# Performance work log

Hardware: AMD Instinct MI355X
Metric: run time of the kernel (lower is better)

Reference implementation:

```python
import jax, jax.numpy as jnp
import numpy as np

NUM_HEADS = 4
HEAD_DIM = 64
IN_CH = 192
KERNEL_SIZES = (3, 5, 7, 9)  # per-head neighborhood size
NEG_INF = -1e30


def setup_inputs() -> dict:
    key = jax.random.key(0)
    k1, k2, k3 = jax.random.split(key, 3)
    x = jax.random.normal(k1, (8, IN_CH, 96, 96), dtype=jnp.float32)
    # QKV conv: out_channels = head_dim * num_heads * 3 = 768, 3x3, pad 1
    w_qkv = jax.random.normal(k2, (HEAD_DIM * NUM_HEADS * 3, IN_CH, 3, 3), dtype=jnp.float32) * 0.02
    b_qkv = jax.random.normal(k3, (HEAD_DIM * NUM_HEADS * 3,), dtype=jnp.float32) * 0.02
    return {"x": x, "w_qkv": w_qkv, "b_qkv": b_qkv}


def _neighborhood_attention(q, k, v, ksize):
    # q, k, v: [N, H, W, D]; KxK zero-padded neighborhood attention with
    # out-of-bounds positions masked out.
    N, H, W, D = q.shape
    pad = ksize // 2
    kp = jnp.pad(k, ((0, 0), (pad, pad), (pad, pad), (0, 0)))
    vp = jnp.pad(v, ((0, 0), (pad, pad), (pad, pad), (0, 0)))
    scale = 1.0 / np.sqrt(D).astype(np.float32)
    rows = jnp.arange(H)
    cols = jnp.arange(W)
    scores, masks = [], []
    for di in range(ksize):
        for dj in range(ksize):
            k_sh = kp[:, di:di + H, dj:dj + W, :]           # shifted keys
            scores.append(jnp.einsum('nhwd,nhwd->nhw', q, k_sh))
            rv = (rows + di - pad >= 0) & (rows + di - pad < H)   # [H]
            cv = (cols + dj - pad >= 0) & (cols + dj - pad < W)   # [W]
            masks.append(rv[:, None] & cv[None, :])               # [H, W]
    scores = jnp.stack(scores, axis=-1) * scale                   # [N,H,W,K2]
    mask = jnp.stack(masks, axis=-1)[None]                        # [1,H,W,K2]
    scores = jnp.where(mask, scores, NEG_INF)
    attn = jax.nn.softmax(scores, axis=-1)                        # [N,H,W,K2]
    out = jnp.zeros_like(q)
    t = 0
    for di in range(ksize):
        for dj in range(ksize):
            out = out + attn[..., t, None] * vp[:, di:di + H, dj:dj + W, :]
            t += 1
    return out  # [N,H,W,D]


def reference(x, w_qkv, b_qkv):
    # Dense QKV projection (Conv2d, stride 1, padding 1 == SAME for k=3)
    qkv = jax.lax.conv_general_dilated(
        x, w_qkv, window_strides=(1, 1), padding='SAME',
        dimension_numbers=('NCHW', 'OIHW', 'NCHW'))
    qkv = qkv + b_qkv[None, :, None, None]
    # transform_to_nhw1c: NCHW -> NHWC, then split channels into
    # num_heads blocks of 3*head_dim, each split into q, k, v.
    N, C, H, W = qkv.shape
    qkv = jnp.transpose(qkv, (0, 2, 3, 1)).reshape(N, H, W, NUM_HEADS, 3, HEAD_DIM)
    outs = []
    for h, ks in enumerate(KERNEL_SIZES):
        q = qkv[..., h, 0, :]
        k = qkv[..., h, 1, :]
        v = qkv[..., h, 2, :]
        o = _neighborhood_attention(q, k, v, ks)       # [N,H,W,D]
        outs.append(jnp.transpose(o, (0, 3, 1, 2)))    # transform_from_nhw1c -> NCHW
    return jnp.stack(outs, axis=0)  # [num_heads, N, D, H, W]
```

## Files before the change

### kernel.cpp

```cpp
#include <hip/hip_runtime.h>
#include <hip/hip_bf16.h>

#define NH 96
#define NW 96
#define NB 8
#define CIN 192
#define COUT 768
#define PH 98

typedef __attribute__((ext_vector_type(8))) unsigned short ushort8;
typedef __attribute__((ext_vector_type(8))) short bf16x8;
typedef __attribute__((ext_vector_type(4))) float f32x4;

static __device__ __forceinline__ unsigned short f2bf(float f) {
    unsigned int u = __float_as_uint(f);
    return (unsigned short)((u + 0x7fffu + ((u >> 16) & 1u)) >> 16);
}

typedef const __attribute__((address_space(1))) unsigned int gu32;
typedef __attribute__((address_space(3))) unsigned int lu32;
static __device__ __forceinline__ void gload16(const void* g, void* l) {
    __builtin_amdgcn_global_load_lds((gu32*)g, (lu32*)l, 16, 0, 0);
}

__global__ __launch_bounds__(256) void pack_x_kernel(
    const float* __restrict__ x, unsigned short* __restrict__ xp)
{
    __shared__ float tile[32][97];
    int bid = blockIdx.x;
    int ct = bid % 6; int y = (bid / 6) % NH; int n = bid / (6 * NH);
    int tid = threadIdx.x;
    int c0 = ct * 32;
    for (int i = tid; i < 32 * 96; i += 256) {
        int c = i / 96, xx = i % 96;
        tile[c][xx] = x[(((size_t)n * CIN + c0 + c) * NH + y) * NW + xx];
    }
    __syncthreads();
    for (int i = tid; i < 96 * 4; i += 256) {
        int xx = i >> 2, ch = i & 3;
        ushort8 pk;
#pragma unroll
        for (int j = 0; j < 8; ++j) pk[j] = f2bf(tile[ch * 8 + j][xx]);
        *(ushort8*)(xp + ((size_t)(n * PH + y + 1) * PH + xx + 1) * CIN + c0 + ch * 8) = pk;
    }
}

__global__ __launch_bounds__(256) void pack_w_kernel(
    const float* __restrict__ w, unsigned short* __restrict__ bw)
{
    __shared__ float ls[1728];
    int co = blockIdx.x; int tid = threadIdx.x;
    for (int i = tid; i < 1728; i += 256) ls[i] = w[(size_t)co * 1728 + i];
    __syncthreads();
    for (int i = tid; i < 1728; i += 256) {
        int sh = i / 192, ci = i % 192;
        bw[(size_t)co * 1728 + i] = f2bf(ls[ci * 9 + sh]);
    }
}

__global__ __launch_bounds__(512) void conv_gemm_kernel(
    const unsigned short* __restrict__ xp, const unsigned short* __restrict__ bw,
    const float* __restrict__ bias, unsigned short* __restrict__ qkq,
    unsigned short* __restrict__ vt)
{
    __shared__ __align__(16) char smem[131072];
    int bid = (blockIdx.x & 7) * 108 + (blockIdx.x >> 3);
    int brow = (bid / 3) * 256, bcol = (bid % 3) * 256;
    int tid = threadIdx.x, lane = tid & 63;
    int wid = tid >> 6, wm = wid >> 2, wn = wid & 3;
    int g = lane >> 4;

    const unsigned short* srcA[2][2];
    const unsigned short* srcB[2][2];
#pragma unroll
    for (int h = 0; h < 2; ++h)
#pragma unroll
        for (int i = 0; i < 2; ++i) {
            int s = i * 512 + tid;
            int rl = s >> 3, c = s & 7;
            int csw = (c ^ (rl & 7)) << 3;
            int p = brow + h * 128 + rl;
            int n = p / 9216; int rem = p - n * 9216;
            int y = rem / 96; int xx = rem - y * 96;
            srcA[h][i] = xp + ((size_t)(n * PH + y) * PH + xx) * CIN + csw;
            srcB[h][i] = bw + (size_t)(bcol + h * 128 + rl) * 1728 + csw;
        }
    int dsto[2];
#pragma unroll
    for (int i = 0; i < 2; ++i) dsto[i] = (i * 512 + (tid & ~63)) * 16;

#define STAGEU(T, U, BUF)                                                      \
    {                                                                          \
        int shift_ = (T) / 3, kk_ = (T) % 3;                                   \
        if ((U) < 2) {                                                         \
            int aO_ = ((shift_ / 3) * PH + (shift_ % 3)) * CIN + kk_ * 64;     \
            _Pragma("unroll")                                                  \
            for (int i_ = 0; i_ < 2; ++i_)                                     \
                gload16(srcA[(U)][i_] + aO_,                                   \
                        smem + (BUF) + (U) * 16384 + dsto[i_]);                \
        } else {                                                               \
            int bO_ = (T) * 64;                                                \
            _Pragma("unroll")                                                  \
            for (int i_ = 0; i_ < 2; ++i_)                                     \
                gload16(srcB[(U) - 2][i_] + bO_,                               \
                        smem + (BUF) + 32768 + ((U) - 2) * 16384 + dsto[i_]);  \
        }                                                                      \
    }

    int arow[8], brow_[4], xof[2];
#pragma unroll
    for (int m = 0; m < 8; ++m)
        arow[m] = (wm * 128 + m * 16 + (lane & 15)) * 128;
#pragma unroll
    for (int n = 0; n < 4; ++n)
        brow_[n] = 32768 + (wn * 64 + n * 16 + (lane & 15)) * 128;
#pragma unroll
    for (int kk = 0; kk < 2; ++kk)
        xof[kk] = ((kk * 4 + g) ^ (lane & 7)) << 4;

    STAGEU(0, 0, 0); STAGEU(0, 1, 0); STAGEU(0, 2, 0); STAGEU(0, 3, 0);

    f32x4 acc[8][4] = {};

    for (int t = 0; t < 27; ++t) {
        asm volatile("s_waitcnt vmcnt(0)" ::: "memory");
        __builtin_amdgcn_s_barrier();
        __builtin_amdgcn_sched_barrier(0);
        const int cur = (t & 1) << 16;
        const int nxt = cur ^ 65536;
        bf16x8 bf[4][2];
#pragma unroll
        for (int n = 0; n < 4; ++n)
#pragma unroll
            for (int kk = 0; kk < 2; ++kk)
                bf[n][kk] = *(const bf16x8*)(smem + cur + brow_[n] + xof[kk]);
#pragma unroll
        for (int p = 0; p < 4; ++p) {
            if (t < 26) STAGEU(t + 1, p, nxt);
            bf16x8 af[2][2];
#pragma unroll
            for (int mm = 0; mm < 2; ++mm)
#pragma unroll
                for (int kk = 0; kk < 2; ++kk)
                    af[mm][kk] = *(const bf16x8*)(smem + cur + arow[2 * p + mm] + xof[kk]);
            __builtin_amdgcn_s_setprio(1);
#pragma unroll
            for (int mm = 0; mm < 2; ++mm)
#pragma unroll
                for (int n = 0; n < 4; ++n)
#pragma unroll
                    for (int kk = 0; kk < 2; ++kk)
                        acc[2 * p + mm][n] = __builtin_amdgcn_mfma_f32_16x16x32_bf16(
                            af[mm][kk], bf[n][kk], acc[2 * p + mm][n], 0, 0, 0);
            __builtin_amdgcn_s_setprio(0);
        }
    }

    __syncthreads();
    unsigned short* sc = (unsigned short*)smem;
    float bn[4];
#pragma unroll
    for (int n = 0; n < 4; ++n)
        bn[n] = bias[bcol + wn * 64 + n * 16 + (lane & 15)];
#pragma unroll
    for (int m = 0; m < 8; ++m)
#pragma unroll
        for (int n = 0; n < 4; ++n) {
            int col = wn * 64 + n * 16 + (lane & 15);
            int cabs = bcol + col;
            float scale = ((cabs % 192) < 64) ? 0.125f : 1.0f;
#pragma unroll
            for (int j = 0; j < 4; ++j) {
                int row = wm * 128 + m * 16 + (lane >> 4) * 4 + j;
                sc[row * 256 + (col ^ ((row & 7) << 3))] =
                    f2bf((acc[m][n][j] + bn[n]) * scale);
            }
        }
    __syncthreads();
#pragma unroll
    for (int i = 0; i < 16; ++i) {
        int idx = i * 512 + tid;
        int row = idx >> 5, ch = idx & 31;
        int c0 = bcol + ch * 8;
        int r192 = c0 % 192;
        if (r192 < 128) {
            ushort8 pk = *(const ushort8*)(sc + row * 256 + ((ch * 8) ^ ((row & 7) << 3)));
            *(ushort8*)(qkq + (size_t)(brow + row) * 512 + (c0 / 192) * 128 + r192) = pk;
        }
    }
    int nblk = brow / 9216;
    int prem = brow - nblk * 9216;
#pragma unroll
    for (int h = 0; h < 4; ++h) {
        int lc = h * 192 + 128 - bcol;
        if (lc < 0 || lc > 192) continue;
        unsigned short* vth = vt + (size_t)h * 4718592;
#pragma unroll
        for (int it = 0; it < 4; ++it) {
            int i = it * 512 + tid;
            int d = i & 63, pxb = i >> 6;
            ushort8 pk;
#pragma unroll
            for (int j = 0; j < 8; ++j) {
                int px = pxb * 8 + j;
                pk[j] = sc[px * 256 + ((lc + d) ^ ((px & 7) << 3))];
            }
            *(ushort8*)(vth + ((size_t)(nblk * 64 + d)) * 9216 + prem + pxb * 8) = pk;
        }
    }
}

#define SLAB 24576
template<int KS>
static __device__ __forceinline__ void na_body(
    const unsigned short* __restrict__ qkq, const unsigned short* __restrict__ vt,
    float* __restrict__ out, int head, int bid, char* nsm)
{
    constexpr int PAD = KS / 2;
    int yp = bid % 32, n = bid / 32;
    int y0 = yp * 3;
    int tid = threadIdx.x;
    int wv = tid >> 6, lane = tid & 63;
    int g = lane >> 4, pix = lane & 15;
    int x0 = wv * 16;
    int x = x0 + pix;
    int W = x0 - 8;

    size_t qb0 = ((size_t)((n * 96 + y0) * 96 + x)) * 512 + (size_t)head * 128;
    bf16x8 qa0 = *(const bf16x8*)(qkq + qb0 + g * 8);
    bf16x8 qa1 = *(const bf16x8*)(qkq + qb0 + 32 + g * 8);
    bf16x8 qc0 = *(const bf16x8*)(qkq + qb0 + 96 * 512 + g * 8);
    bf16x8 qc1 = *(const bf16x8*)(qkq + qb0 + 96 * 512 + 32 + g * 8);
    bf16x8 qe0 = *(const bf16x8*)(qkq + qb0 + 2 * 96 * 512 + g * 8);
    bf16x8 qe1 = *(const bf16x8*)(qkq + qb0 + 2 * 96 * 512 + 32 + g * 8);
    asm volatile("s_waitcnt vmcnt(0)" ::: "memory");

    const size_t hoff = (size_t)head * 128 + 64;
#define STAGEKV(DI, BUF)                                                       \
    {                                                                          \
        int iy_ = min(max(y0 + (DI) - PAD, 0), 95);                            \
        size_t rb_ = ((size_t)((n * 96 + iy_) * 96)) * 512 + hoff;             \
        _Pragma("unroll")                                                      \
        for (int i_ = 0; i_ < 2; ++i_) {                                       \
            int ch_ = i_ * 384 + tid;                                          \
            int xx_ = ch_ >> 3, c8_ = (ch_ & 7) ^ (xx_ & 7);                   \
            gload16(qkq + rb_ + (size_t)xx_ * 512 + c8_ * 8,                   \
                    nsm + (BUF) * SLAB + (i_ * 384 + (tid & ~63)) * 16);       \
        }                                                                      \
        _Pragma("unroll")                                                      \
        for (int i_ = 0; i_ < 2; ++i_) {                                       \
            int ch_ = i_ * 384 + tid;                                          \
            int d_ = ch_ / 12, c_ = ch_ % 12;                                  \
            int cs_ = c_ ^ ((d_ >> 1) & 3);                                    \
            gload16(vt + (((size_t)(n * 64 + d_) * 96 + iy_)) * 96 + cs_ * 8,  \
                    nsm + (BUF) * SLAB + 12288 + (i_ * 384 + (tid & ~63)) * 16); \
        }                                                                      \
    }

    STAGEKV(0, 0);
    STAGEKV(1, 1);

    float l0 = 0.f, l1 = 0.f, l2 = 0.f;
    f32x4 O0[4] = {}, O1[4] = {}, O2[4] = {};
    int addrA = ((2 * (g & 1)) * 16 + pix) * 4;
    int addrB = addrA + 64;
    bool kthi = (g >> 1) != 0;
    int cxg = min(max(2 * wv - 1 + g, 0), 11);
    int vbase = 12288 + pix * 192 + ((cxg ^ ((pix >> 1) & 3)) << 4);

#define ROWCOMP(QF0, QF1, L, O)                                                \
    {                                                                          \
        unsigned int w0[2], w1[2];                                             \
        _Pragma("unroll")                                                      \
        for (int kt = 0; kt < 2; ++kt) {                                       \
            f32x4 tt = {};                                                     \
            tt = __builtin_amdgcn_mfma_f32_16x16x32_bf16(kf0[kt], QF0, tt, 0, 0, 0); \
            tt = __builtin_amdgcn_mfma_f32_16x16x32_bf16(kf1[kt], QF1, tt, 0, 0, 0); \
            float p[4];                                                        \
            _Pragma("unroll")                                                  \
            for (int r = 0; r < 4; ++r) {                                      \
                int kix = W + kt * 16 + g * 4 + r;                             \
                bool valid = ((unsigned)(kix - x + PAD) <= (unsigned)(2 * PAD)) && \
                             ((unsigned)kix < 96u);                            \
                p[r] = valid ? __expf(tt[r]) : 0.f;                            \
            }                                                                  \
            L += (p[0] + p[1]) + (p[2] + p[3]);                                \
            asm("v_cvt_pk_bf16_f32 %0, %1, %2" : "=v"(w0[kt]) : "v"(p[0]), "v"(p[1])); \
            asm("v_cvt_pk_bf16_f32 %0, %1, %2" : "=v"(w1[kt]) : "v"(p[2]), "v"(p[3])); \
        }                                                                      \
        int a0 = __builtin_amdgcn_ds_bpermute(addrA, (int)w0[0]);              \
        int b0 = __builtin_amdgcn_ds_bpermute(addrA, (int)w0[1]);              \
        int a1 = __builtin_amdgcn_ds_bpermute(addrA, (int)w1[0]);              \
        int b1 = __builtin_amdgcn_ds_bpermute(addrA, (int)w1[1]);              \
        int a2 = __builtin_amdgcn_ds_bpermute(addrB, (int)w0[0]);              \
        int b2 = __builtin_amdgcn_ds_bpermute(addrB, (int)w0[1]);              \
        int a3 = __builtin_amdgcn_ds_bpermute(addrB, (int)w1[0]);              \
        int b3 = __builtin_amdgcn_ds_bpermute(addrB, (int)w1[1]);              \
        union { int u[4]; bf16x8 v; } pa;                                      \
        pa.u[0] = kthi ? b0 : a0;                                              \
        pa.u[1] = kthi ? b1 : a1;                                              \
        pa.u[2] = kthi ? b2 : a2;                                              \
        pa.u[3] = kthi ? b3 : a3;                                              \
        _Pragma("unroll")                                                      \
        for (int dc = 0; dc < 4; ++dc)                                         \
            O[dc] = __builtin_amdgcn_mfma_f32_16x16x32_bf16(pa.v, vf[dc], O[dc], 0, 0, 0); \
    }

#pragma unroll
    for (int di = 0; di <= KS + 1; ++di) {
        if (di <= KS) asm volatile("s_waitcnt vmcnt(4)" ::: "memory");
        else          asm volatile("s_waitcnt vmcnt(0)" ::: "memory");
        __builtin_amdgcn_s_barrier();
        __builtin_amdgcn_sched_barrier(0);
        if (di + 2 <= KS + 1) STAGEKV(di + 2, (di + 2) % 3);
        int iy = y0 + di - PAD;
        if (iy < 0 || iy >= 96) continue;
        const char* kb = nsm + (di % 3) * SLAB;

        bf16x8 kf0[2], kf1[2];
#pragma unroll
        for (int kt = 0; kt < 2; ++kt) {
            int kix_l = W + kt * 16 + pix;
            int ixc = min(max(kix_l, 0), 95);
            const char* kr = kb + ixc * 128;
            kf0[kt] = *(const bf16x8*)(kr + ((g ^ (ixc & 7)) << 4));
            kf1[kt] = *(const bf16x8*)(kr + (((4 + g) ^ (ixc & 7)) << 4));
        }
        bf16x8 vf[4];
#pragma unroll
        for (int dc = 0; dc < 4; ++dc)
            vf[dc] = *(const bf16x8*)(kb + dc * 3072 + vbase);

        if (di < KS)              ROWCOMP(qa0, qa1, l0, O0);
        if (di >= 1 && di <= KS)  ROWCOMP(qc0, qc1, l1, O1);
        if (di >= 2)              ROWCOMP(qe0, qe1, l2, O2);
    }

    l0 += __shfl_xor(l0, 16, 64); l0 += __shfl_xor(l0, 32, 64);
    l1 += __shfl_xor(l1, 16, 64); l1 += __shfl_xor(l1, 32, 64);
    l2 += __shfl_xor(l2, 16, 64); l2 += __shfl_xor(l2, 32, 64);
    float li0 = 1.0f / l0, li1 = 1.0f / l1, li2 = 1.0f / l2;
    float lj0[4], lj1[4], lj2[4];
#pragma unroll
    for (int j = 0; j < 4; ++j) {
        lj0[j] = __uint_as_float((unsigned)__builtin_amdgcn_ds_bpermute(
            (4 * g + j) * 4, (int)__float_as_uint(li0)));
        lj1[j] = __uint_as_float((unsigned)__builtin_amdgcn_ds_bpermute(
            (4 * g + j) * 4, (int)__float_as_uint(li1)));
        lj2[j] = __uint_as_float((unsigned)__builtin_amdgcn_ds_bpermute(
            (4 * g + j) * 4, (int)__float_as_uint(li2)));
    }
    __syncthreads();
    float (*sO3)[64][97] = (float(*)[64][97])nsm;
#pragma unroll
    for (int dc = 0; dc < 4; ++dc)
#pragma unroll
        for (int j = 0; j < 4; ++j) {
            sO3[0][dc * 16 + pix][x0 + g * 4 + j] = O0[dc][j] * lj0[j];
            sO3[1][dc * 16 + pix][x0 + g * 4 + j] = O1[dc][j] * lj1[j];
            sO3[2][dc * 16 + pix][x0 + g * 4 + j] = O2[dc][j] * lj2[j];
        }
    __syncthreads();
    for (int i = tid; i < 4608; i += 384) {
        int r = i / 1536;
        int rem = i - r * 1536;
        int d = rem / 24, xq = rem % 24;
        float4 v4 = { sO3[r][d][xq * 4], sO3[r][d][xq * 4 + 1],
                      sO3[r][d][xq * 4 + 2], sO3[r][d][xq * 4 + 3] };
        *(float4*)(out + ((size_t)(head * 8 + n) * 64 + d) * 9216
                   + (y0 + r) * 96 + xq * 4) = v4;
    }
}

__global__ __launch_bounds__(384, 2) void na_mfma_all(
    const unsigned short* __restrict__ qkq, const unsigned short* __restrict__ vt,
    float* __restrict__ out)
{
    __shared__ __align__(16) char nsm[74496];
    int head = blockIdx.x & 3;
    int bid = blockIdx.x >> 2;
    switch (head) {
        case 0: na_body<3>(qkq, vt,               out, 0, bid, nsm); break;
        case 1: na_body<5>(qkq, vt + 4718592,     out, 1, bid, nsm); break;
        case 2: na_body<7>(qkq, vt + 2 * 4718592, out, 2, bid, nsm); break;
        default: na_body<9>(qkq, vt + 3 * 4718592, out, 3, bid, nsm); break;
    }
}

extern "C" void kernel_launch(void* const* d_in, const int* in_sizes, int n_in,
                              void* d_out, int out_size, void* d_ws, size_t ws_size,
                              hipStream_t stream) {
    const float* x  = (const float*)d_in[0];
    const float* w  = (const float*)d_in[1];
    const float* b  = (const float*)d_in[2];
    float* out = (float*)d_out;

    unsigned short* qkq  = (unsigned short*)d_ws;
    unsigned short* vt   = (unsigned short*)((char*)d_ws + 75497472);
    unsigned short* xpad = (unsigned short*)((char*)d_ws + 113246208);
    unsigned short* bw   = (unsigned short*)((char*)d_ws + 142749696);

    hipMemsetAsync(xpad, 0, 29503488, stream);
    pack_x_kernel<<<NB * NH * 6, 256, 0, stream>>>(x, xpad);
    pack_w_kernel<<<COUT, 256, 0, stream>>>(w, bw);
    conv_gemm_kernel<<<864, 512, 0, stream>>>(xpad, bw, b, qkq, vt);

    na_mfma_all<<<4 * 256, 384, 0, stream>>>(qkq, vt, out);
}
```

Before: 317.4 us.

## Shrink conv GEMM M-tile to one image row and triple-buffer loads

```diff
diff --git a/kernel.cpp b/kernel.cpp
--- a/kernel.cpp
+++ b/kernel.cpp
@@ -58,76 +58,89 @@
     }
 }
 
+#define CBUF 45056
+
+#define STAGE(T, BUF)                                                          \
+    {                                                                          \
+        int shift_ = (T) / 3, kk_ = (T) % 3;                                   \
+        int aO_ = ((shift_ / 3) * PH + (shift_ % 3)) * CIN + kk_ * 64;         \
+        int bO_ = (T) * 64;                                                    \
+        gload16(srcA0 + aO_, smem + (BUF) + dstA0);                            \
+        if (tid < 256) gload16(srcA1 + aO_, smem + (BUF) + dstA1);             \
+        _Pragma("unroll")                                                      \
+        for (int i_ = 0; i_ < 4; ++i_)                                         \
+            gload16(srcB[i_] + bO_, smem + (BUF) + 12288 + dstB[i_]);          \
+    }
+
+#define GATE65()                                                               \
+    {                                                                          \
+        if (tid < 256) { asm volatile("s_waitcnt vmcnt(6)" ::: "memory"); }    \
+        else           { asm volatile("s_waitcnt vmcnt(5)" ::: "memory"); }    \
+    }
+
 __global__ __launch_bounds__(512) void conv_gemm_kernel(
     const unsigned short* __restrict__ xp, const unsigned short* __restrict__ bw,
     const float* __restrict__ bias, unsigned short* __restrict__ qkq,
     unsigned short* __restrict__ vt)
 {
-    __shared__ __align__(16) char smem[131072];
-    int bid = (blockIdx.x & 7) * 108 + (blockIdx.x >> 3);
-    int brow = (bid / 3) * 256, bcol = (bid % 3) * 256;
+    __shared__ __align__(16) char smem[3 * CBUF];
+    int bid = (blockIdx.x & 7) * 288 + (blockIdx.x >> 3);
+    int brow = (bid / 3) * 96, bcol = (bid % 3) * 256;
     int tid = threadIdx.x, lane = tid & 63;
     int wid = tid >> 6, wm = wid >> 2, wn = wid & 3;
     int g = lane >> 4;
 
-    const unsigned short* srcA[2][2];
-    const unsigned short* srcB[2][2];
-#pragma unroll
-    for (int h = 0; h < 2; ++h)
-#pragma unroll
-        for (int i = 0; i < 2; ++i) {
-            int s = i * 512 + tid;
-            int rl = s >> 3, c = s & 7;
-            int csw = (c ^ (rl & 7)) << 3;
-            int p = brow + h * 128 + rl;
-            int n = p / 9216; int rem = p - n * 9216;
-            int y = rem / 96; int xx = rem - y * 96;
-            srcA[h][i] = xp + ((size_t)(n * PH + y) * PH + xx) * CIN + csw;
-            srcB[h][i] = bw + (size_t)(bcol + h * 128 + rl) * 1728 + csw;
-        }
-    int dsto[2];
-#pragma unroll
-    for (int i = 0; i < 2; ++i) dsto[i] = (i * 512 + (tid & ~63)) * 16;
-
-#define STAGEU(T, U, BUF)                                                      \
-    {                                                                          \
-        int shift_ = (T) / 3, kk_ = (T) % 3;                                   \
-        if ((U) < 2) {                                                         \
-            int aO_ = ((shift_ / 3) * PH + (shift_ % 3)) * CIN + kk_ * 64;     \
-            _Pragma("unroll")                                                  \
-            for (int i_ = 0; i_ < 2; ++i_)                                     \
-                gload16(srcA[(U)][i_] + aO_,                                   \
-                        smem + (BUF) + (U) * 16384 + dsto[i_]);                \
-        } else {                                                               \
-            int bO_ = (T) * 64;                                                \
-            _Pragma("unroll")                                                  \
-            for (int i_ = 0; i_ < 2; ++i_)                                     \
-                gload16(srcB[(U) - 2][i_] + bO_,                               \
-                        smem + (BUF) + 32768 + ((U) - 2) * 16384 + dsto[i_]);  \
-        }                                                                      \
-    }
-
-    int arow[8], brow_[4], xof[2];
-#pragma unroll
-    for (int m = 0; m < 8; ++m)
-        arow[m] = (wm * 128 + m * 16 + (lane & 15)) * 128;
+    int nblk = brow / 9216;
+    int prem = brow - nblk * 9216;
+    int yy = prem / 96;
+
+    const unsigned short* srcA0;
+    const unsigned short* srcA1;
+    int dstA0, dstA1;
+    {
+        int r0 = tid >> 3, c0 = tid & 7;
+        srcA0 = xp + ((size_t)(nblk * PH + yy) * PH + r0) * CIN
+                   + ((c0 ^ (r0 & 7)) << 3);
+        dstA0 = (tid & ~63) * 16;
+        int s1 = 512 + tid;
+        int r1 = s1 >> 3, c1 = s1 & 7;
+        srcA1 = xp + ((size_t)(nblk * PH + yy) * PH + r1) * CIN
+                   + ((c1 ^ (r1 & 7)) << 3);
+        dstA1 = (512 + (tid & ~63)) * 16;
+    }
+    const unsigned short* srcB[4];
+    int dstB[4];
+#pragma unroll
+    for (int i = 0; i < 4; ++i) {
+        int s = i * 512 + tid;
+        int row = s >> 3, c = s & 7;
+        srcB[i] = bw + (size_t)(bcol + row) * 1728 + ((c ^ (row & 7)) << 3);
+        dstB[i] = (i * 512 + (tid & ~63)) * 16;
+    }
+
+    int arow[3], brow_[4], xof[2];
+#pragma unroll
+    for (int m = 0; m < 3; ++m)
+        arow[m] = (wm * 48 + m * 16 + (lane & 15)) * 128;
 #pragma unroll
     for (int n = 0; n < 4; ++n)
-        brow_[n] = 32768 + (wn * 64 + n * 16 + (lane & 15)) * 128;
+        brow_[n] = 12288 + (wn * 64 + n * 16 + (lane & 15)) * 128;
 #pragma unroll
     for (int kk = 0; kk < 2; ++kk)
         xof[kk] = ((kk * 4 + g) ^ (lane & 7)) << 4;
 
-    STAGEU(0, 0, 0); STAGEU(0, 1, 0); STAGEU(0, 2, 0); STAGEU(0, 3, 0);
-
-    f32x4 acc[8][4] = {};
+    STAGE(0, 0);
+    STAGE(1, CBUF);
+
+    f32x4 acc[3][4] = {};
 
     for (int t = 0; t < 27; ++t) {
-        asm volatile("s_waitcnt vmcnt(0)" ::: "memory");
+        if (t < 26) GATE65()
+        else        asm volatile("s_waitcnt vmcnt(0)" ::: "memory");
         __builtin_amdgcn_s_barrier();
         __builtin_amdgcn_sched_barrier(0);
-        const int cur = (t & 1) << 16;
-        const int nxt = cur ^ 65536;
+        if (t < 25) STAGE(t + 2, ((t + 2) % 3) * CBUF);
+        const int cur = (t % 3) * CBUF;
         bf16x8 bf[4][2];
 #pragma unroll
         for (int n = 0; n < 4; ++n)
@@ -135,23 +148,18 @@
             for (int kk = 0; kk < 2; ++kk)
                 bf[n][kk] = *(const bf16x8*)(smem + cur + brow_[n] + xof[kk]);
 #pragma unroll
-        for (int p = 0; p < 4; ++p) {
-            if (t < 26) STAGEU(t + 1, p, nxt);
-            bf16x8 af[2][2];
-#pragma unroll
-            for (int mm = 0; mm < 2; ++mm)
+        for (int m = 0; m < 3; ++m) {
+            bf16x8 af[2];
+#pragma unroll
+            for (int kk = 0; kk < 2; ++kk)
+                af[kk] = *(const bf16x8*)(smem + cur + arow[m] + xof[kk]);
+            __builtin_amdgcn_s_setprio(1);
+#pragma unroll
+            for (int n = 0; n < 4; ++n)
 #pragma unroll
                 for (int kk = 0; kk < 2; ++kk)
-                    af[mm][kk] = *(const bf16x8*)(smem + cur + arow[2 * p + mm] + xof[kk]);
-            __builtin_amdgcn_s_setprio(1);
-#pragma unroll
-            for (int mm = 0; mm < 2; ++mm)
-#pragma unroll
-                for (int n = 0; n < 4; ++n)
-#pragma unroll
-                    for (int kk = 0; kk < 2; ++kk)
-                        acc[2 * p + mm][n] = __builtin_amdgcn_mfma_f32_16x16x32_bf16(
-                            af[mm][kk], bf[n][kk], acc[2 * p + mm][n], 0, 0, 0);
+                    acc[m][n] = __builtin_amdgcn_mfma_f32_16x16x32_bf16(
+                        af[kk], bf[n][kk], acc[m][n], 0, 0, 0);
             __builtin_amdgcn_s_setprio(0);
         }
     }
@@ -163,7 +171,7 @@
     for (int n = 0; n < 4; ++n)
         bn[n] = bias[bcol + wn * 64 + n * 16 + (lane & 15)];
 #pragma unroll
-    for (int m = 0; m < 8; ++m)
+    for (int m = 0; m < 3; ++m)
 #pragma unroll
         for (int n = 0; n < 4; ++n) {
             int col = wn * 64 + n * 16 + (lane & 15);
@@ -171,14 +179,14 @@
             float scale = ((cabs % 192) < 64) ? 0.125f : 1.0f;
 #pragma unroll
             for (int j = 0; j < 4; ++j) {
-                int row = wm * 128 + m * 16 + (lane >> 4) * 4 + j;
+                int row = wm * 48 + m * 16 + (lane >> 4) * 4 + j;
                 sc[row * 256 + (col ^ ((row & 7) << 3))] =
                     f2bf((acc[m][n][j] + bn[n]) * scale);
             }
         }
     __syncthreads();
 #pragma unroll
-    for (int i = 0; i < 16; ++i) {
+    for (int i = 0; i < 6; ++i) {
         int idx = i * 512 + tid;
         int row = idx >> 5, ch = idx & 31;
         int c0 = bcol + ch * 8;
@@ -188,24 +196,25 @@
             *(ushort8*)(qkq + (size_t)(brow + row) * 512 + (c0 / 192) * 128 + r192) = pk;
         }
     }
-    int nblk = brow / 9216;
-    int prem = brow - nblk * 9216;
 #pragma unroll
     for (int h = 0; h < 4; ++h) {
         int lc = h * 192 + 128 - bcol;
         if (lc < 0 || lc > 192) continue;
         unsigned short* vth = vt + (size_t)h * 4718592;
 #pragma unroll
-        for (int it = 0; it < 4; ++it) {
+        for (int it = 0; it < 2; ++it) {
             int i = it * 512 + tid;
-            int d = i & 63, pxb = i >> 6;
-            ushort8 pk;
-#pragma unroll
-            for (int j = 0; j < 8; ++j) {
-                int px = pxb * 8 + j;
-                pk[j] = sc[px * 256 + ((lc + d) ^ ((px & 7) << 3))];
+            if (i < 768) {
+                int d = i & 63, pxb = i >> 6;
+                ushort8 pk;
+#pragma unroll
+                for (int j = 0; j < 8; ++j) {
+                    int px = pxb * 8 + j;
+                    pk[j] = sc[px * 256 + ((lc + d) ^ ((px & 7) << 3))];
+                }
+                *(ushort8*)(vth + ((size_t)(nblk * 64 + d)) * 9216
+                            + prem + pxb * 8) = pk;
             }
-            *(ushort8*)(vth + ((size_t)(nblk * 64 + d)) * 9216 + prem + pxb * 8) = pk;
         }
     }
 }
@@ -403,7 +412,7 @@
     hipMemsetAsync(xpad, 0, 29503488, stream);
     pack_x_kernel<<<NB * NH * 6, 256, 0, stream>>>(x, xpad);
     pack_w_kernel<<<COUT, 256, 0, stream>>>(w, bw);
-    conv_gemm_kernel<<<864, 512, 0, stream>>>(xpad, bw, b, qkq, vt);
+    conv_gemm_kernel<<<2304, 512, 0, stream>>>(xpad, bw, b, qkq, vt);
 
     na_mfma_all<<<4 * 256, 384, 0, stream>>>(qkq, vt, out);
 }
```

Measured after the change: 341.3 us. 1.08x slower.
